# Optimization experiments

Measured on AMD Instinct MI355X. Metric: run time of the kernel, lower is better.

The kernel has to match this reference:

```python
import jax, jax.numpy as jnp
import numpy as np

LEVEL = 3
NUM_BANDS = LEVEL + 1
B, N, D_MODEL, PATCH_NUMS, PRED_LEN = 32, 7, 768, 64, 336

# db4 lowpass decomposition filter (pywt convention)
_DB4_DEC_LO = np.array([
    -0.010597401784997278, 0.032883011666982945, 0.030841381835986965,
    -0.18703481171888114, -0.02798376941698385, 0.6308807679295904,
    0.7148465705525415, 0.23037781330885523], dtype=np.float32)
REC_LO = _DB4_DEC_LO[::-1].copy()                                   # reconstruction lowpass
REC_HI = (_DB4_DEC_LO * ((-1.0) ** (np.arange(8) + 1))).astype(np.float32)  # reconstruction highpass (QMF)


def _upsample2(x):
    # zero-interleave along last axis: (..., L) -> (..., 2L)
    z = jnp.zeros_like(x)
    return jnp.stack([x, z], axis=-1).reshape(*x.shape[:-1], 2 * x.shape[-1])


def _idwt_per(ca, cd, rec_lo, rec_hi):
    # single-level inverse DWT, periodization mode, along last axis: (..., L) -> (..., 2L)
    F = rec_lo.shape[0]
    ua, ud = _upsample2(ca), _upsample2(cd)
    y = jnp.zeros_like(ua)
    for k in range(F):  # small fixed tap loop (F=8)
        y = y + jnp.roll(ua, k, axis=-1) * rec_lo[k] + jnp.roll(ud, k, axis=-1) * rec_hi[k]
    return jnp.roll(y, -(F // 2 - 1), axis=-1)  # compensate filter delay


def _iswt(coeffs, level, rec_lo, rec_hi):
    # coeffs: (..., T, level+1) with bands ordered [cA, cD_level, ..., cD1]
    T = coeffs.shape[-2]
    out = coeffs[..., 0]
    for j in range(level, 0, -1):
        step = 2 ** (j - 1)
        cd = coeffs[..., level - j + 1]
        M = T // step
        # gather the `step` interleaved subsequences as a batch axis: (..., step, M)
        o = jnp.moveaxis(out.reshape(*out.shape[:-1], M, step), -1, -2)
        d = jnp.moveaxis(cd.reshape(*cd.shape[:-1], M, step), -1, -2)
        x1 = _idwt_per(o[..., 0::2], d[..., 0::2], rec_lo, rec_hi)
        x2 = jnp.roll(_idwt_per(o[..., 1::2], d[..., 1::2], rec_lo, rec_hi), 1, axis=-1)
        new = 0.5 * (x1 + x2)  # (..., step, M)
        out = jnp.moveaxis(new, -2, -1).reshape(*out.shape[:-1], T)
    return out


def setup_inputs() -> dict:
    key = jax.random.key(0)
    kx, kw, kb = jax.random.split(key, 3)
    Din = D_MODEL * PATCH_NUMS
    x = jax.random.normal(kx, (B, N, D_MODEL, PATCH_NUMS), dtype=jnp.float32)
    # Linear init ~ U(-1/sqrt(Din), 1/sqrt(Din)); small normal is equivalent for a reference
    W = jax.random.normal(kw, (NUM_BANDS, Din, PRED_LEN), dtype=jnp.float32) * (1.0 / np.sqrt(Din))
    b = jax.random.normal(kb, (NUM_BANDS, PRED_LEN), dtype=jnp.float32) * 0.01
    return {"x": x, "W": W, "b": b}


def reference(x, W, b):
    # x: (B, N, d_model, patch_nums); W: (bands, d_model*patch_nums, pred_len); b: (bands, pred_len)
    Bb, Nn, dm, P = x.shape
    xf = x.reshape(Bb, Nn, dm * P)  # Flatten(start_dim=-2)
    # all band projections as one batched GEMM -> (B, N, pred_len, bands)
    coeffs = jnp.einsum('bnd,kdp->bnpk', xf, W) + b.T
    rec_lo = jnp.asarray(REC_LO)
    rec_hi = jnp.asarray(REC_HI)
    return _iswt(coeffs, LEVEL, rec_lo, rec_hi)  # (B, N, pred_len)
```

## Files before the change

kernel.cpp:

```cpp
#include <hip/hip_runtime.h>
#include <hip/hip_bf16.h>
#include <stdint.h>

#define M_ROWS   224
#define K_DIM    49152
#define NCOL     1344
#define PRED     336
#define S_CHUNKS 36
#define KSTEPS   1536
#define LDA      40

typedef __attribute__((ext_vector_type(8))) short short8;
typedef __attribute__((ext_vector_type(4))) short short4_t;
typedef __attribute__((ext_vector_type(4))) float floatx4;

__device__ __forceinline__ uint16_t f32_to_bf16(float f) {
    uint32_t u = __builtin_bit_cast(uint32_t, f);
    uint32_t r = (u + 0x7fffu + ((u >> 16) & 1u)) >> 16;
    return (uint16_t)r;
}
__device__ __forceinline__ float bf16_to_f32(uint16_t h) {
    uint32_t u = ((uint32_t)h) << 16;
    return __builtin_bit_cast(float, u);
}

__global__ __launch_bounds__(256, 3) void gemm_partial(
    const float* __restrict__ X,
    const float* __restrict__ W,
    uint16_t* __restrict__ P)
{
    __shared__ uint16_t lA[M_ROWS * LDA];

    const int ct   = blockIdx.x;
    const int s    = blockIdx.y;
    const int tid  = threadIdx.x;
    const int lane = tid & 63;
    const int w    = tid >> 6;
    const int c0w  = ct * 64 + w * 16;
    const int band = c0w / PRED;
    const int p0   = c0w - band * PRED;
    const int l15  = lane & 15;
    const int kq   = lane >> 4;

    const float* wbase = W + (size_t)band * ((size_t)K_DIM * PRED)
                           + (size_t)(kq * 8) * PRED
                           + (size_t)(p0 + l15);

    const int step_begin = (s * KSTEPS) / S_CHUNKS;
    const int step_end   = ((s + 1) * KSTEPS) / S_CHUNKS;

    floatx4 acc[14];
    #pragma unroll
    for (int f = 0; f < 14; ++f) acc[f] = (floatx4){0.f, 0.f, 0.f, 0.f};

    for (int st = step_begin; st < step_end; ++st) {
        const int k0 = st * 32;

        const float* wp = wbase + (size_t)k0 * PRED;
        float bf[8];
        #pragma unroll
        for (int j = 0; j < 8; ++j) bf[j] = wp[(size_t)j * PRED];

        __syncthreads();

        #pragma unroll
        for (int r = 0; r < 7; ++r) {
            const int i     = tid + 256 * r;
            const int m     = i >> 3;
            const int piece = i & 7;
            const float4 v = *((const float4*)(X + (size_t)m * K_DIM + k0) + piece);
            short4_t pk;
            pk.x = (short)f32_to_bf16(v.x);
            pk.y = (short)f32_to_bf16(v.y);
            pk.z = (short)f32_to_bf16(v.z);
            pk.w = (short)f32_to_bf16(v.w);
            *(short4_t*)&lA[m * LDA + piece * 4] = pk;
        }
        __syncthreads();

        short8 bfrag;
        #pragma unroll
        for (int j = 0; j < 4; ++j) {
            ((uint32_t*)&bfrag)[j] =
                (uint32_t)f32_to_bf16(bf[2 * j]) | ((uint32_t)f32_to_bf16(bf[2 * j + 1]) << 16);
        }

        #pragma unroll
        for (int f = 0; f < 14; ++f) {
            short8 afrag = *(const short8*)&lA[(16 * f + l15) * LDA + kq * 8];
            acc[f] = __builtin_amdgcn_mfma_f32_16x16x32_bf16(afrag, bfrag, acc[f], 0, 0, 0);
        }
    }

    const int col = c0w + l15;
    #pragma unroll
    for (int f = 0; f < 14; ++f) {
        #pragma unroll
        for (int r = 0; r < 4; ++r) {
            const int m = 16 * f + kq * 4 + r;
            P[((size_t)m * S_CHUNKS + s) * NCOL + col] = f32_to_bf16(acc[f][r]);
        }
    }
}

__device__ const float REC_LO[8] = {
     0.23037781330885523f,  0.7148465705525415f,   0.6308807679295904f,
    -0.02798376941698385f, -0.18703481171888114f,  0.030841381835986965f,
     0.032883011666982945f, -0.010597401784997278f };
__device__ const float REC_HI[8] = {
     0.010597401784997278f, 0.032883011666982945f, -0.030841381835986965f,
    -0.18703481171888114f,  0.02798376941698385f,   0.6308807679295904f,
    -0.7148465705525415f,   0.23037781330885523f };

__global__ __launch_bounds__(256) void reduce_iswt(
    const uint16_t* __restrict__ P,
    const float* __restrict__ bias,
    float* __restrict__ out)
{
    __shared__ float coeff[NCOL];
    __shared__ float buf[2][PRED];

    const int row = blockIdx.x;
    const int tid = threadIdx.x;
    const uint16_t* pr = P + (size_t)row * S_CHUNKS * NCOL;

    for (int c = tid; c < NCOL; c += 256) {
        float a = bias[c];
        for (int s = 0; s < S_CHUNKS; ++s) a += bf16_to_f32(pr[s * NCOL + c]);
        coeff[c] = a;
    }
    __syncthreads();

    for (int t = tid; t < PRED; t += 256) buf[0][t] = coeff[t];
    __syncthreads();

    int curb = 0;
    for (int j = 3; j >= 1; --j) {
        const int step = 1 << (j - 1);
        const int M    = PRED / step;
        const float* cd  = &coeff[(4 - j) * PRED];
        const float* cur = buf[curb];
        float* nxt       = buf[curb ^ 1];
        for (int t = tid; t < PRED; t += 256) {
            const int s = t & (step - 1);
            const int m = t / step;
            const int mm1 = (m == 0) ? (M - 1) : (m - 1);
            float x1 = 0.f, x2 = 0.f;
            #pragma unroll
            for (int k = 0; k < 8; ++k) {
                int i1 = m + 3 - k;  if (i1 < 0) i1 += M; else if (i1 >= M) i1 -= M;
                if ((i1 & 1) == 0) {
                    const int pos = i1 * step + s;
                    x1 += cur[pos] * REC_LO[k] + cd[pos] * REC_HI[k];
                }
                int i2 = mm1 + 3 - k;  if (i2 < 0) i2 += M; else if (i2 >= M) i2 -= M;
                if ((i2 & 1) == 0) {
                    const int pos = (i2 + 1) * step + s;
                    x2 += cur[pos] * REC_LO[k] + cd[pos] * REC_HI[k];
                }
            }
            nxt[t] = 0.5f * (x1 + x2);
        }
        __syncthreads();
        curb ^= 1;
    }

    for (int t = tid; t < PRED; t += 256) out[(size_t)row * PRED + t] = buf[curb][t];
}

extern "C" void kernel_launch(void* const* d_in, const int* in_sizes, int n_in,
                              void* d_out, int out_size, void* d_ws, size_t ws_size,
                              hipStream_t stream) {
    const float* X    = (const float*)d_in[0];
    const float* W    = (const float*)d_in[1];
    const float* bias = (const float*)d_in[2];
    float* out        = (float*)d_out;
    uint16_t* P       = (uint16_t*)d_ws;

    gemm_partial<<<dim3(21, S_CHUNKS), 256, 0, stream>>>(X, W, P);
    reduce_iswt<<<M_ROWS, 256, 0, stream>>>(P, bias, out);
}
```

Before: 435.4 us.

## Pre-convert X to bf16 and stream A tiles via global_load_lds with prefetch

Adds a separate kernel that converts X to bf16 once into workspace, so each GEMM block no longer reloads fp32 X and converts it per k-step. The GEMM now moves A tiles straight into LDS with global_load_lds in an MFMA-fragment layout and prefetches the next W fragment and A tile while current MFMAs run. The reduce kernel reads packed bf16 pairs and uses 1024 threads so each column is handled by one thread. This costs an extra kernel launch and a bf16 copy of X in workspace at a fixed offset, which relies on the workspace being large enough.

```diff
diff --git a/kernel.cpp b/kernel.cpp
--- a/kernel.cpp
+++ b/kernel.cpp
@@ -1,5 +1,4 @@
 #include <hip/hip_runtime.h>
-#include <hip/hip_bf16.h>
 #include <stdint.h>
 
 #define M_ROWS   224
@@ -8,10 +7,10 @@
 #define PRED     336
 #define S_CHUNKS 36
 #define KSTEPS   1536
-#define LDA      40
+
+#define XB_OFFSET (32u * 1024u * 1024u)
 
 typedef __attribute__((ext_vector_type(8))) short short8;
-typedef __attribute__((ext_vector_type(4))) short short4_t;
 typedef __attribute__((ext_vector_type(4))) float floatx4;
 
 __device__ __forceinline__ uint16_t f32_to_bf16(float f) {
@@ -23,29 +22,48 @@
     uint32_t u = ((uint32_t)h) << 16;
     return __builtin_bit_cast(float, u);
 }
+__device__ __forceinline__ uint32_t pack2(float lo, float hi) {
+    return (uint32_t)f32_to_bf16(lo) | ((uint32_t)f32_to_bf16(hi) << 16);
+}
+
+__global__ __launch_bounds__(256) void cvt_x(
+    const float* __restrict__ X, uint16_t* __restrict__ Xb)
+{
+    const size_t i = ((size_t)blockIdx.x * 256 + threadIdx.x) * 8;
+    const float4 a = *(const float4*)(X + i);
+    const float4 b = *(const float4*)(X + i + 4);
+    uint4 o;
+    o.x = pack2(a.x, a.y);
+    o.y = pack2(a.z, a.w);
+    o.z = pack2(b.x, b.y);
+    o.w = pack2(b.z, b.w);
+    *(uint4*)(Xb + i) = o;
+}
 
 __global__ __launch_bounds__(256, 3) void gemm_partial(
-    const float* __restrict__ X,
+    const uint16_t* __restrict__ Xb,
     const float* __restrict__ W,
     uint16_t* __restrict__ P)
 {
-    __shared__ uint16_t lA[M_ROWS * LDA];
+    __shared__ uint16_t lA[M_ROWS * 32];
 
     const int ct   = blockIdx.x;
     const int s    = blockIdx.y;
     const int tid  = threadIdx.x;
     const int lane = tid & 63;
     const int w    = tid >> 6;
+    const int l15  = lane & 15;
+    const int kq   = lane >> 4;
     const int c0w  = ct * 64 + w * 16;
     const int band = c0w / PRED;
     const int p0   = c0w - band * PRED;
-    const int l15  = lane & 15;
-    const int kq   = lane >> 4;
 
     const float* wbase = W + (size_t)band * ((size_t)K_DIM * PRED)
                            + (size_t)(kq * 8) * PRED
                            + (size_t)(p0 + l15);
 
+    const size_t grow = (size_t)l15 * K_DIM + (size_t)kq * 8;
+
     const int step_begin = (s * KSTEPS) / S_CHUNKS;
     const int step_end   = ((s + 1) * KSTEPS) / S_CHUNKS;
 
@@ -53,43 +71,66 @@
     #pragma unroll
     for (int f = 0; f < 14; ++f) acc[f] = (floatx4){0.f, 0.f, 0.f, 0.f};
 
+    float wcur[8], wnxt[8];
+
+    {
+        const float* wp = wbase + (size_t)(step_begin * 32) * PRED;
+        #pragma unroll
+        for (int j = 0; j < 8; ++j) wcur[j] = wp[(size_t)j * PRED];
+
+        const int k0 = step_begin * 32;
+        #pragma unroll
+        for (int r = 0; r < 4; ++r) {
+            const int f = w + 4 * r;
+            if (f < 14) {
+                const uint16_t* gp = Xb + (size_t)(16 * f) * K_DIM + grow + k0;
+                __builtin_amdgcn_global_load_lds(
+                    (const __attribute__((address_space(1))) void*)gp,
+                    (__attribute__((address_space(3))) void*)&lA[f * 512],
+                    16, 0, 0);
+            }
+        }
+    }
+
     for (int st = step_begin; st < step_end; ++st) {
-        const int k0 = st * 32;
-
-        const float* wp = wbase + (size_t)k0 * PRED;
-        float bf[8];
-        #pragma unroll
-        for (int j = 0; j < 8; ++j) bf[j] = wp[(size_t)j * PRED];
-
         __syncthreads();
 
-        #pragma unroll
-        for (int r = 0; r < 7; ++r) {
-            const int i     = tid + 256 * r;
-            const int m     = i >> 3;
-            const int piece = i & 7;
-            const float4 v = *((const float4*)(X + (size_t)m * K_DIM + k0) + piece);
-            short4_t pk;
-            pk.x = (short)f32_to_bf16(v.x);
-            pk.y = (short)f32_to_bf16(v.y);
-            pk.z = (short)f32_to_bf16(v.z);
-            pk.w = (short)f32_to_bf16(v.w);
-            *(short4_t*)&lA[m * LDA + piece * 4] = pk;
-        }
+        short8 bfrag;
+        #pragma unroll
+        for (int j = 0; j < 4; ++j)
+            ((uint32_t*)&bfrag)[j] = pack2(wcur[2 * j], wcur[2 * j + 1]);
+
+        {
+            const int stn = (st + 1 < step_end) ? st + 1 : st;
+            const float* wp = wbase + (size_t)(stn * 32) * PRED;
+            #pragma unroll
+            for (int j = 0; j < 8; ++j) wnxt[j] = wp[(size_t)j * PRED];
+        }
+
+        #pragma unroll
+        for (int f = 0; f < 14; ++f) {
+            short8 afrag = *(const short8*)&lA[f * 512 + lane * 8];
+            acc[f] = __builtin_amdgcn_mfma_f32_16x16x32_bf16(afrag, bfrag, acc[f], 0, 0, 0);
+        }
+
         __syncthreads();
 
-        short8 bfrag;
-        #pragma unroll
-        for (int j = 0; j < 4; ++j) {
-            ((uint32_t*)&bfrag)[j] =
-                (uint32_t)f32_to_bf16(bf[2 * j]) | ((uint32_t)f32_to_bf16(bf[2 * j + 1]) << 16);
-        }
-
-        #pragma unroll
-        for (int f = 0; f < 14; ++f) {
-            short8 afrag = *(const short8*)&lA[(16 * f + l15) * LDA + kq * 8];
-            acc[f] = __builtin_amdgcn_mfma_f32_16x16x32_bf16(afrag, bfrag, acc[f], 0, 0, 0);
-        }
+        if (st + 1 < step_end) {
+            const int k0 = (st + 1) * 32;
+            #pragma unroll
+            for (int r = 0; r < 4; ++r) {
+                const int f = w + 4 * r;
+                if (f < 14) {
+                    const uint16_t* gp = Xb + (size_t)(16 * f) * K_DIM + grow + k0;
+                    __builtin_amdgcn_global_load_lds(
+                        (const __attribute__((address_space(1))) void*)gp,
+                        (__attribute__((address_space(3))) void*)&lA[f * 512],
+                        16, 0, 0);
+                }
+            }
+        }
+        #pragma unroll
+        for (int j = 0; j < 8; ++j) wcur[j] = wnxt[j];
     }
 
     const int col = c0w + l15;
@@ -112,7 +153,7 @@
     -0.18703481171888114f,  0.02798376941698385f,   0.6308807679295904f,
     -0.7148465705525415f,   0.23037781330885523f };
 
-__global__ __launch_bounds__(256) void reduce_iswt(
+__global__ __launch_bounds__(1024) void reduce_iswt(
     const uint16_t* __restrict__ P,
     const float* __restrict__ bias,
     float* __restrict__ out)
@@ -122,16 +163,22 @@
 
     const int row = blockIdx.x;
     const int tid = threadIdx.x;
-    const uint16_t* pr = P + (size_t)row * S_CHUNKS * NCOL;
-
-    for (int c = tid; c < NCOL; c += 256) {
-        float a = bias[c];
-        for (int s = 0; s < S_CHUNKS; ++s) a += bf16_to_f32(pr[s * NCOL + c]);
-        coeff[c] = a;
+    const uint32_t* pr = (const uint32_t*)(P + (size_t)row * S_CHUNKS * NCOL);
+
+    if (tid < NCOL / 2) {
+        float a0 = 0.f, a1 = 0.f;
+        #pragma unroll 4
+        for (int s = 0; s < S_CHUNKS; ++s) {
+            const uint32_t v = pr[s * (NCOL / 2) + tid];
+            a0 += bf16_to_f32((uint16_t)(v & 0xffff));
+            a1 += bf16_to_f32((uint16_t)(v >> 16));
+        }
+        coeff[2 * tid]     = a0 + bias[2 * tid];
+        coeff[2 * tid + 1] = a1 + bias[2 * tid + 1];
     }
     __syncthreads();
 
-    for (int t = tid; t < PRED; t += 256) buf[0][t] = coeff[t];
+    if (tid < PRED) buf[0][tid] = coeff[tid];
     __syncthreads();
 
     int curb = 0;
@@ -141,7 +188,8 @@
         const float* cd  = &coeff[(4 - j) * PRED];
         const float* cur = buf[curb];
         float* nxt       = buf[curb ^ 1];
-        for (int t = tid; t < PRED; t += 256) {
+        if (tid < PRED) {
+            const int t = tid;
             const int s = t & (step - 1);
             const int m = t / step;
             const int mm1 = (m == 0) ? (M - 1) : (m - 1);
@@ -165,7 +213,7 @@
         curb ^= 1;
     }
 
-    for (int t = tid; t < PRED; t += 256) out[(size_t)row * PRED + t] = buf[curb][t];
+    if (tid < PRED) out[(size_t)row * PRED + tid] = buf[curb][tid];
 }
 
 extern "C" void kernel_launch(void* const* d_in, const int* in_sizes, int n_in,
@@ -176,7 +224,9 @@
     const float* bias = (const float*)d_in[2];
     float* out        = (float*)d_out;
     uint16_t* P       = (uint16_t*)d_ws;
-
-    gemm_partial<<<dim3(21, S_CHUNKS), 256, 0, stream>>>(X, W, P);
-    reduce_iswt<<<M_ROWS, 256, 0, stream>>>(P, bias, out);
-}
+    uint16_t* Xb      = (uint16_t*)((char*)d_ws + XB_OFFSET);
+
+    cvt_x       <<<5376, 256, 0, stream>>>(X, Xb);
+    gemm_partial<<<dim3(21, S_CHUNKS), 256, 0, stream>>>(Xb, W, P);
+    reduce_iswt <<<M_ROWS, 1024, 0, stream>>>(P, bias, out);
+}
```

Result: no change. 438.1 us (+0.6%).
